# Performance work log

Measured on AMD Instinct MI355X. Metric: run time of the kernel, lower is better.

## Reference

```python
import jax, jax.numpy as jnp
import numpy as np
import math

D_MODEL = 1024
NUM_HEADS = 16
HEAD_DIM = D_MODEL // NUM_HEADS


def _xavier(key, out_f, in_f):
    limit = math.sqrt(6.0 / (in_f + out_f))
    return jax.random.uniform(key, (out_f, in_f), jnp.float32, -limit, limit)


def ternarize(w):
    # abs-mean threshold -> {-1, 0, +1}
    abs_mean = jnp.mean(jnp.abs(w))
    return jnp.where(jnp.abs(w) > abs_mean, jnp.sign(w), jnp.zeros_like(w))


def setup_inputs() -> dict:
    key = jax.random.key(0)
    kq, kk, kv, kwq, kwk, kwv, kwo = jax.random.split(key, 7)
    B, S = 2, 2048
    return {
        "query": jax.random.normal(kq, (B, S, D_MODEL), jnp.float32),
        "key": jax.random.normal(kk, (B, S, D_MODEL), jnp.float32),
        "value": jax.random.normal(kv, (B, S, D_MODEL), jnp.float32),
        "w_q": _xavier(kwq, D_MODEL, D_MODEL),
        "w_k": _xavier(kwk, D_MODEL, D_MODEL),
        "w_v": _xavier(kwv, D_MODEL, D_MODEL),
        "w_o": _xavier(kwo, D_MODEL, D_MODEL),
    }


def reference(query, key, value, w_q, w_k, w_v, w_o):
    B, S, _ = query.shape
    # ternary projections (F.linear: x @ W.T)
    q = query @ ternarize(w_q).T
    k = key @ ternarize(w_k).T
    v = value @ ternarize(w_v).T
    # [B, H, S, Dh]
    q = q.reshape(B, S, NUM_HEADS, HEAD_DIM).transpose(0, 2, 1, 3)
    k = k.reshape(B, -1, NUM_HEADS, HEAD_DIM).transpose(0, 2, 1, 3)
    v = v.reshape(B, -1, NUM_HEADS, HEAD_DIM).transpose(0, 2, 1, 3)
    scores = jnp.einsum("bhqd,bhkd->bhqk", q, k) / math.sqrt(HEAD_DIM)
    probs = jax.nn.softmax(scores, axis=-1)
    out = jnp.einsum("bhqk,bhkd->bhqd", probs, v)
    out = out.transpose(0, 2, 1, 3).reshape(B, S, D_MODEL)
    return out @ ternarize(w_o).T
```

## Files before the change

### kernel.cpp

```cpp
#include <hip/hip_runtime.h>
#include <cstdint>
#include <cstddef>

typedef __bf16 bfloat;
typedef __bf16 bf16x8 __attribute__((ext_vector_type(8)));
typedef __bf16 bf16x4 __attribute__((ext_vector_type(4)));
typedef float  f32x4  __attribute__((ext_vector_type(4)));

static constexpr int D  = 1024;
static constexpr int S  = 2048;
static constexpr int B  = 2;
static constexpr int H  = 16;
static constexpr int DH = 64;
static constexpr int M  = B * S;
static constexpr int WMAT_N = 1024 * 1024;

#define MFMA_BF16(a, b, c) __builtin_amdgcn_mfma_f32_16x16x32_bf16((a), (b), (c), 0, 0, 0)

__device__ __forceinline__ void gl_lds16(const void* g, void* l) {
  __builtin_amdgcn_global_load_lds(
      (const __attribute__((address_space(1))) void*)g,
      (__attribute__((address_space(3))) void*)l, 16, 0, 0);
}

__global__ void absum_kernel(const float* __restrict__ w0, const float* __restrict__ w1,
                             const float* __restrict__ w2, const float* __restrict__ w3,
                             double* __restrict__ sums) {
  int z = blockIdx.y;
  const float* w = (z == 0) ? w0 : (z == 1) ? w1 : (z == 2) ? w2 : w3;
  const float4* w4 = (const float4*)w;
  double s = 0.0;
  for (int i = blockIdx.x * blockDim.x + threadIdx.x; i < (WMAT_N / 4);
       i += gridDim.x * blockDim.x) {
    float4 v = w4[i];
    s += (double)fabsf(v.x) + (double)fabsf(v.y) + (double)fabsf(v.z) + (double)fabsf(v.w);
  }
  for (int off = 1; off < 64; off <<= 1) s += __shfl_xor(s, off, 64);
  __shared__ double ps[4];
  if ((threadIdx.x & 63) == 0) ps[threadIdx.x >> 6] = s;
  __syncthreads();
  if (threadIdx.x == 0) atomicAdd(&sums[z], ps[0] + ps[1] + ps[2] + ps[3]);
}

__global__ void tern_kernel(const float* __restrict__ w0, const float* __restrict__ w1,
                            const float* __restrict__ w2, const float* __restrict__ w3,
                            bfloat* __restrict__ o0, bfloat* __restrict__ o1,
                            bfloat* __restrict__ o2, bfloat* __restrict__ o3,
                            const double* __restrict__ sums) {
  int z = blockIdx.y;
  const float* w = (z == 0) ? w0 : (z == 1) ? w1 : (z == 2) ? w2 : w3;
  bfloat* o = (z == 0) ? o0 : (z == 1) ? o1 : (z == 2) ? o2 : o3;
  double thr = sums[z] * (1.0 / (double)WMAT_N);
  const float4* w4 = (const float4*)w;
  for (int i = blockIdx.x * blockDim.x + threadIdx.x; i < (WMAT_N / 4);
       i += gridDim.x * blockDim.x) {
    float4 v = w4[i];
    bf16x4 r;
    r[0] = (bfloat)(((double)fabsf(v.x) > thr) ? (v.x > 0.f ? 1.f : -1.f) : 0.f);
    r[1] = (bfloat)(((double)fabsf(v.y) > thr) ? (v.y > 0.f ? 1.f : -1.f) : 0.f);
    r[2] = (bfloat)(((double)fabsf(v.z) > thr) ? (v.z > 0.f ? 1.f : -1.f) : 0.f);
    r[3] = (bfloat)(((double)fabsf(v.w) > thr) ? (v.w > 0.f ? 1.f : -1.f) : 0.f);
    *(bf16x4*)&o[(size_t)i * 4] = r;
  }
}

__global__ void splitcvt3_kernel(const float* __restrict__ qx, const float* __restrict__ kx,
                                 const float* __restrict__ vx, bfloat* __restrict__ qhi,
                                 bfloat* __restrict__ qlo, bfloat* __restrict__ khi,
                                 bfloat* __restrict__ klo, bfloat* __restrict__ vhi) {
  int z = blockIdx.y;
  const float* x = (z == 0) ? qx : (z == 1) ? kx : vx;
  bfloat* hi = (z == 0) ? qhi : (z == 1) ? khi : vhi;
  bfloat* lo = (z == 0) ? qlo : (z == 1) ? klo : nullptr;
  const int n4 = M * D / 4;
  const float4* x4 = (const float4*)x;
  for (int i = blockIdx.x * blockDim.x + threadIdx.x; i < n4; i += gridDim.x * blockDim.x) {
    float4 v = x4[i];
    bf16x4 h;
    h[0] = (bfloat)v.x; h[1] = (bfloat)v.y; h[2] = (bfloat)v.z; h[3] = (bfloat)v.w;
    *(bf16x4*)&hi[(size_t)i * 4] = h;
    if (z < 2) {
      bf16x4 l;
      l[0] = (bfloat)(v.x - (float)h[0]);
      l[1] = (bfloat)(v.y - (float)h[1]);
      l[2] = (bfloat)(v.z - (float)h[2]);
      l[3] = (bfloat)(v.w - (float)h[3]);
      *(bf16x4*)&lo[(size_t)i * 4] = l;
    }
  }
}

__global__ __launch_bounds__(256) void transpose_v(const bfloat* __restrict__ in,
                                                   bfloat* __restrict__ out) {
  __shared__ __align__(16) bfloat T[64 * 72];
  const int t = threadIdx.x;
  const int s0 = blockIdx.x * 64, n0 = blockIdx.y * 64, b = blockIdx.z;
#pragma unroll
  for (int p = 0; p < 2; p++) {
    int e = t * 8 + p * 2048;
    int r = e >> 6, cc = e & 63;
    bf16x8 v = *(const bf16x8*)&in[(size_t)(b * S + s0 + r) * D + n0 + cc];
#pragma unroll
    for (int j = 0; j < 8; j++) T[(cc + j) * 72 + r] = v[j];
  }
  __syncthreads();
#pragma unroll
  for (int p = 0; p < 2; p++) {
    int e = t * 8 + p * 2048;
    int f = e >> 6, cc = e & 63;
    bf16x8 v = *(const bf16x8*)&T[f * 72 + cc];
    *(bf16x8*)&out[(size_t)b * D * S + (size_t)(n0 + f) * S + s0 + cc] = v;
  }
}

__global__ __launch_bounds__(256) void qkv_gemm(
    const bfloat* __restrict__ xqh, const bfloat* __restrict__ xql,
    const bfloat* __restrict__ xkh, const bfloat* __restrict__ xkl,
    const bfloat* __restrict__ xvh, const bfloat* __restrict__ wqt,
    const bfloat* __restrict__ wkt, const bfloat* __restrict__ wvt,
    bfloat* __restrict__ qmh, bfloat* __restrict__ qml,
    bfloat* __restrict__ kmh, bfloat* __restrict__ kml, bfloat* __restrict__ vmm) {
  constexpr int K = D;
  constexpr int N = D;
  __shared__ __align__(16) bfloat As0[128 * 32];
  __shared__ __align__(16) bfloat As1[128 * 32];
  __shared__ __align__(16) bfloat Ws[128 * 32];

  const int z = blockIdx.z;
  const bfloat *A0, *A1 = nullptr, *Wm;
  bfloat *Oh, *Ol = nullptr;
  float scale = 1.f;
  bool split;
  if (z == 0) {
    A0 = xqh; A1 = xql; Wm = wqt; Oh = qmh; Ol = qml;
    scale = 0.18033688f;
    split = true;
  } else if (z == 1) {
    A0 = xkh; A1 = xkl; Wm = wkt; Oh = kmh; Ol = kml; split = true;
  } else {
    A0 = xvh; Wm = wvt; Oh = vmm; split = false;
  }

  const int t = threadIdx.x;
  const int w = t >> 6, lane = t & 63;
  const int quad = lane >> 4, l16 = lane & 15;
  const int wm = w >> 1, wn = w & 1;
  const int m0 = blockIdx.y * 128, n0 = blockIdx.x * 128;

  f32x4 acc[4][4] = {};

  const int sr = t >> 2;
  const int sc = (t & 3) * 8;

  const bfloat* pA0a = A0 + (size_t)(m0 + sr) * K + sc;
  const bfloat* pA0b = A0 + (size_t)(m0 + 64 + sr) * K + sc;
  const bfloat* pA1a = split ? A1 + (size_t)(m0 + sr) * K + sc : nullptr;
  const bfloat* pA1b = split ? A1 + (size_t)(m0 + 64 + sr) * K + sc : nullptr;
  const bfloat* pWa = Wm + (size_t)(n0 + sr) * K + sc;
  const bfloat* pWb = Wm + (size_t)(n0 + 64 + sr) * K + sc;

  for (int kk = 0; kk < K; kk += 32) {
    gl_lds16(pA0a + kk, As0 + w * 512);
    gl_lds16(pA0b + kk, As0 + 2048 + w * 512);
    if (split) {
      gl_lds16(pA1a + kk, As1 + w * 512);
      gl_lds16(pA1b + kk, As1 + 2048 + w * 512);
    }
    gl_lds16(pWa + kk, Ws + w * 512);
    gl_lds16(pWb + kk, Ws + 2048 + w * 512);
    __syncthreads();

    bf16x8 bfrag[4], afrag[4];
#pragma unroll
    for (int nt = 0; nt < 4; nt++)
      bfrag[nt] = *(const bf16x8*)&Ws[(wn * 64 + nt * 16 + l16) * 32 + quad * 8];
#pragma unroll
    for (int mt = 0; mt < 4; mt++)
      afrag[mt] = *(const bf16x8*)&As0[(wm * 64 + mt * 16 + l16) * 32 + quad * 8];
#pragma unroll
    for (int mt = 0; mt < 4; mt++)
#pragma unroll
      for (int nt = 0; nt < 4; nt++)
        acc[mt][nt] = MFMA_BF16(afrag[mt], bfrag[nt], acc[mt][nt]);
    if (split) {
#pragma unroll
      for (int mt = 0; mt < 4; mt++)
        afrag[mt] = *(const bf16x8*)&As1[(wm * 64 + mt * 16 + l16) * 32 + quad * 8];
#pragma unroll
      for (int mt = 0; mt < 4; mt++)
#pragma unroll
        for (int nt = 0; nt < 4; nt++)
          acc[mt][nt] = MFMA_BF16(afrag[mt], bfrag[nt], acc[mt][nt]);
    }
    __syncthreads();
  }

#pragma unroll
  for (int mt = 0; mt < 4; mt++) {
#pragma unroll
    for (int nt = 0; nt < 4; nt++) {
      const int row = m0 + wm * 64 + mt * 16 + quad * 4;
      const int col = n0 + wn * 64 + nt * 16 + l16;
#pragma unroll
      for (int rg = 0; rg < 4; rg++) {
        float vv = acc[mt][nt][rg] * scale;
        size_t idx = (size_t)(row + rg) * N + col;
        bfloat hh = (bfloat)vv;
        Oh[idx] = hh;
        if (split) Ol[idx] = (bfloat)(vv - (float)hh);
      }
    }
  }
}

__global__ __launch_bounds__(256) void gemm_wo(const bfloat* __restrict__ A,
                                               const bfloat* __restrict__ Wm,
                                               float* __restrict__ Cf) {
  constexpr int K = D;
  constexpr int N = D;
  __shared__ __align__(16) bfloat As[128 * 32];
  __shared__ __align__(16) bfloat Ws[64 * 32];

  const int t = threadIdx.x;
  const int w = t >> 6, lane = t & 63;
  const int quad = lane >> 4, l16 = lane & 15;
  const int wm = w >> 1, wn = w & 1;
  const int m0 = blockIdx.y * 128, n0 = blockIdx.x * 64;

  f32x4 acc[4][2] = {};

  const int sr = t >> 2;
  const int sc = (t & 3) * 8;
  const bfloat* pAa = A + (size_t)(m0 + sr) * K + sc;
  const bfloat* pAb = A + (size_t)(m0 + 64 + sr) * K + sc;
  const bfloat* pW = Wm + (size_t)(n0 + sr) * K + sc;

  for (int kk = 0; kk < K; kk += 32) {
    gl_lds16(pAa + kk, As + w * 512);
    gl_lds16(pAb + kk, As + 2048 + w * 512);
    gl_lds16(pW + kk, Ws + w * 512);
    __syncthreads();

    bf16x8 bfrag[2], afrag[4];
#pragma unroll
    for (int nt = 0; nt < 2; nt++)
      bfrag[nt] = *(const bf16x8*)&Ws[(wn * 32 + nt * 16 + l16) * 32 + quad * 8];
#pragma unroll
    for (int mt = 0; mt < 4; mt++)
      afrag[mt] = *(const bf16x8*)&As[(wm * 64 + mt * 16 + l16) * 32 + quad * 8];
#pragma unroll
    for (int mt = 0; mt < 4; mt++)
#pragma unroll
      for (int nt = 0; nt < 2; nt++)
        acc[mt][nt] = MFMA_BF16(afrag[mt], bfrag[nt], acc[mt][nt]);
    __syncthreads();
  }

#pragma unroll
  for (int mt = 0; mt < 4; mt++) {
#pragma unroll
    for (int nt = 0; nt < 2; nt++) {
      const int row = m0 + wm * 64 + mt * 16 + quad * 4;
      const int col = n0 + wn * 32 + nt * 16 + l16;
#pragma unroll
      for (int rg = 0; rg < 4; rg++) Cf[(size_t)(row + rg) * N + col] = acc[mt][nt][rg];
    }
  }
}

__global__ __launch_bounds__(256, 4) void flash_kernel(
    const bfloat* __restrict__ qh, const bfloat* __restrict__ ql,
    const bfloat* __restrict__ kh, const bfloat* __restrict__ kl,
    const bfloat* __restrict__ vt, bfloat* __restrict__ outp) {
  __shared__ __align__(16) bfloat Kh[64 * 64];
  __shared__ __align__(16) bfloat Kl[64 * 64];
  __shared__ __align__(16) bfloat Vt[80 * 64];
  __shared__ __align__(16) bfloat Pm[64 * 64];

  const int t = threadIdx.x;
  const int w = t >> 6, lane = t & 63;
  const int quad = lane >> 4, l16 = lane & 15;
  const int b = blockIdx.z, h = blockIdx.y;
  const int q0 = blockIdx.x * 64;
  const size_t base = (size_t)b * S * D + (size_t)h * DH;
  const size_t vbase = (size_t)b * D * S + (size_t)h * DH * S;

  const int ssr = lane >> 3;
  const int spc = lane & 7;

  {
    bf16x4 one = {(bfloat)1.f, (bfloat)1.f, (bfloat)1.f, (bfloat)1.f};
    *(bf16x4*)&Vt[64 * 64 + t * 4] = one;
  }
#pragma unroll
  for (int g = 0; g < 2; g++) {
    int r = w * 16 + g * 8 + ssr;
    int c = spc ^ (r & 7);
    int lo = (w * 16 + g * 8) * 64;
    gl_lds16(qh + base + (size_t)(q0 + r) * D + c * 8, Kh + lo);
    gl_lds16(ql + base + (size_t)(q0 + r) * D + c * 8, Kl + lo);
  }
  __syncthreads();
  bf16x8 ah[2], al[2];
  {
    int row = w * 16 + l16;
#pragma unroll
    for (int s2 = 0; s2 < 2; s2++) {
      ah[s2] = *(const bf16x8*)&Kh[row * 64 + (((s2 * 4 + quad) ^ (row & 7)) * 8)];
      al[s2] = *(const bf16x8*)&Kl[row * 64 + (((s2 * 4 + quad) ^ (row & 7)) * 8)];
    }
  }

  f32x4 Oa[4] = {};
  f32x4 La = {};
  float m_i[4];
#pragma unroll
  for (int i = 0; i < 4; i++) m_i[i] = -3.0e38f;

  for (int k0 = 0; k0 < S; k0 += 64) {
    __syncthreads();
#pragma unroll
    for (int g = 0; g < 2; g++) {
      int r = w * 16 + g * 8 + ssr;
      int c = spc ^ (r & 7);
      int lo = (w * 16 + g * 8) * 64;
      gl_lds16(kh + base + (size_t)(k0 + r) * D + c * 8, Kh + lo);
      gl_lds16(kl + base + (size_t)(k0 + r) * D + c * 8, Kl + lo);
      gl_lds16(vt + vbase + (size_t)r * S + k0 + c * 8, Vt + lo);
    }
    __syncthreads();

    f32x4 sf[4];
#pragma unroll
    for (int nt = 0; nt < 4; nt++) {
      f32x4 acc = {};
      int row = nt * 16 + l16;
#pragma unroll
      for (int s2 = 0; s2 < 2; s2++) {
        bf16x8 bh = *(const bf16x8*)&Kh[row * 64 + (((s2 * 4 + quad) ^ (row & 7)) * 8)];
        bf16x8 bl = *(const bf16x8*)&Kl[row * 64 + (((s2 * 4 + quad) ^ (row & 7)) * 8)];
        acc = MFMA_BF16(ah[s2], bh, acc);
        acc = MFMA_BF16(al[s2], bh, acc);
        acc = MFMA_BF16(ah[s2], bl, acc);
      }
      sf[nt] = acc;
    }

#pragma unroll
    for (int rg = 0; rg < 4; rg++) {
      float mm = fmaxf(fmaxf(sf[0][rg], sf[1][rg]), fmaxf(sf[2][rg], sf[3][rg]));
#pragma unroll
      for (int off = 1; off < 16; off <<= 1) mm = fmaxf(mm, __shfl_xor(mm, off, 64));
      float mnew = fmaxf(m_i[rg], mm);
      float alpha = exp2f(m_i[rg] - mnew);
      m_i[rg] = mnew;
#pragma unroll
      for (int nt = 0; nt < 4; nt++) sf[nt][rg] = exp2f(sf[nt][rg] - mnew);
#pragma unroll
      for (int nt = 0; nt < 4; nt++) Oa[nt][rg] *= alpha;
      La[rg] *= alpha;
    }

#pragma unroll
    for (int nt = 0; nt < 4; nt++)
#pragma unroll
      for (int rg = 0; rg < 4; rg++) {
        int row = w * 16 + quad * 4 + rg;
        int col = nt * 16 + l16;
        Pm[row * 64 + (((col >> 3) ^ (row & 7)) * 8) + (col & 7)] = (bfloat)sf[nt][rg];
      }

    int prow = w * 16 + l16;
#pragma unroll
    for (int s2 = 0; s2 < 2; s2++) {
      bf16x8 pa = *(const bf16x8*)&Pm[prow * 64 + (((s2 * 4 + quad) ^ (prow & 7)) * 8)];
#pragma unroll
      for (int nt = 0; nt < 4; nt++) {
        int vrow = nt * 16 + l16;
        bf16x8 vb = *(const bf16x8*)&Vt[vrow * 64 + (((s2 * 4 + quad) ^ (vrow & 7)) * 8)];
        Oa[nt] = MFMA_BF16(pa, vb, Oa[nt]);
      }
      bf16x8 vb1 = *(const bf16x8*)&Vt[(64 + l16) * 64 + (((s2 * 4 + quad) ^ (l16 & 7)) * 8)];
      La = MFMA_BF16(pa, vb1, La);
    }
  }

#pragma unroll
  for (int rg = 0; rg < 4; rg++) {
    float inv = 1.0f / La[rg];
#pragma unroll
    for (int nt = 0; nt < 4; nt++) {
      outp[base + (size_t)(q0 + w * 16 + quad * 4 + rg) * D + nt * 16 + l16] =
          (bfloat)(Oa[nt][rg] * inv);
    }
  }
}

extern "C" void kernel_launch(void* const* d_in, const int* in_sizes, int n_in,
                              void* d_out, int out_size, void* d_ws, size_t ws_size,
                              hipStream_t stream) {
  const float* q_in = (const float*)d_in[0];
  const float* k_in = (const float*)d_in[1];
  const float* v_in = (const float*)d_in[2];
  const float* wq = (const float*)d_in[3];
  const float* wk = (const float*)d_in[4];
  const float* wv = (const float*)d_in[5];
  const float* wo = (const float*)d_in[6];
  float* outp = (float*)d_out;
  char* ws = (char*)d_ws;

  constexpr size_t WBYTES = (size_t)WMAT_N * 2;
  constexpr size_t XBYTES = (size_t)M * D * 2;
  size_t off = 0;
  double* sums = (double*)(ws + off); off += 256;
  bfloat* wqt = (bfloat*)(ws + off); off += WBYTES;
  bfloat* wkt = (bfloat*)(ws + off); off += WBYTES;
  bfloat* wvt = (bfloat*)(ws + off); off += WBYTES;
  bfloat* wot = (bfloat*)(ws + off); off += WBYTES;
  bfloat* xqh = (bfloat*)(ws + off); off += XBYTES;
  bfloat* xql = (bfloat*)(ws + off); off += XBYTES;
  bfloat* xkh = (bfloat*)(ws + off); off += XBYTES;
  bfloat* xkl = (bfloat*)(ws + off); off += XBYTES;
  bfloat* xvh = (bfloat*)(ws + off); off += XBYTES;
  bfloat* qmh = (bfloat*)(ws + off); off += XBYTES;
  bfloat* qml = (bfloat*)(ws + off); off += XBYTES;
  bfloat* kmh = (bfloat*)(ws + off); off += XBYTES;
  bfloat* kml = (bfloat*)(ws + off); off += XBYTES;
  bfloat* vmm = (bfloat*)(ws + off); off += XBYTES;
  bfloat* attn = xqh;
  bfloat* vtr = xvh;

  hipMemsetAsync(sums, 0, 4 * sizeof(double), stream);
  absum_kernel<<<dim3(128, 4), 256, 0, stream>>>(wq, wk, wv, wo, sums);
  tern_kernel<<<dim3(128, 4), 256, 0, stream>>>(wq, wk, wv, wo, wqt, wkt, wvt, wot, sums);
  splitcvt3_kernel<<<dim3(512, 3), 256, 0, stream>>>(q_in, k_in, v_in, xqh, xql, xkh, xkl, xvh);
  qkv_gemm<<<dim3(D / 128, M / 128, 3), 256, 0, stream>>>(
      xqh, xql, xkh, xkl, xvh, wqt, wkt, wvt, qmh, qml, kmh, kml, vmm);
  transpose_v<<<dim3(S / 64, D / 64, B), 256, 0, stream>>>(vmm, vtr);
  flash_kernel<<<dim3(S / 64, H, B), 256, 0, stream>>>(qmh, qml, kmh, kml, vtr, attn);
  gemm_wo<<<dim3(D / 64, M / 128), 256, 0, stream>>>(attn, wot, outp);
}
```

Baseline: 328.7 us.

## Process 128 query rows per flash block, with DPP row-max and a register ones vector

The flash attention block now covers 128 query rows, two 16-row tiles per wave, so each K/V tile loaded into LDS is reused across twice as many queries. The row-max reduction uses DPP swizzles instead of __shfl_xor, and the row-sum MFMA takes an all-ones operand from a register rather than extra LDS rows. The barrier moves to the end of the loop and launch_bounds drops the occupancy hint. In exchange the grid is half as large (512 blocks) and each thread holds more registers, which may lower occupancy.

Result: slower. 337.0 us (+2.5%).

```diff
diff --git a/kernel.cpp b/kernel.cpp
--- a/kernel.cpp
+++ b/kernel.cpp
@@ -21,6 +21,23 @@
   __builtin_amdgcn_global_load_lds(
       (const __attribute__((address_space(1))) void*)g,
       (__attribute__((address_space(3))) void*)l, 16, 0, 0);
+}
+
+__device__ __forceinline__ float dpp_max16(float x) {
+  float y;
+  y = __builtin_bit_cast(float, __builtin_amdgcn_update_dpp(
+          0, __builtin_bit_cast(int, x), 0xB1, 0xF, 0xF, true));
+  x = fmaxf(x, y);
+  y = __builtin_bit_cast(float, __builtin_amdgcn_update_dpp(
+          0, __builtin_bit_cast(int, x), 0x4E, 0xF, 0xF, true));
+  x = fmaxf(x, y);
+  y = __builtin_bit_cast(float, __builtin_amdgcn_update_dpp(
+          0, __builtin_bit_cast(int, x), 0x141, 0xF, 0xF, true));
+  x = fmaxf(x, y);
+  y = __builtin_bit_cast(float, __builtin_amdgcn_update_dpp(
+          0, __builtin_bit_cast(int, x), 0x140, 0xF, 0xF, true));
+  x = fmaxf(x, y);
+  return x;
 }
 
 __global__ void absum_kernel(const float* __restrict__ w0, const float* __restrict__ w1,
@@ -268,57 +285,66 @@
   }
 }
 
-__global__ __launch_bounds__(256, 4) void flash_kernel(
+__global__ __launch_bounds__(256) void flash_kernel(
     const bfloat* __restrict__ qh, const bfloat* __restrict__ ql,
     const bfloat* __restrict__ kh, const bfloat* __restrict__ kl,
     const bfloat* __restrict__ vt, bfloat* __restrict__ outp) {
   __shared__ __align__(16) bfloat Kh[64 * 64];
   __shared__ __align__(16) bfloat Kl[64 * 64];
-  __shared__ __align__(16) bfloat Vt[80 * 64];
-  __shared__ __align__(16) bfloat Pm[64 * 64];
+  __shared__ __align__(16) bfloat Vt[64 * 64];
+  __shared__ __align__(16) bfloat Pm[128 * 64];
 
   const int t = threadIdx.x;
   const int w = t >> 6, lane = t & 63;
   const int quad = lane >> 4, l16 = lane & 15;
   const int b = blockIdx.z, h = blockIdx.y;
-  const int q0 = blockIdx.x * 64;
+  const int q0 = blockIdx.x * 128;
   const size_t base = (size_t)b * S * D + (size_t)h * DH;
   const size_t vbase = (size_t)b * D * S + (size_t)h * DH * S;
 
   const int ssr = lane >> 3;
   const int spc = lane & 7;
 
-  {
-    bf16x4 one = {(bfloat)1.f, (bfloat)1.f, (bfloat)1.f, (bfloat)1.f};
-    *(bf16x4*)&Vt[64 * 64 + t * 4] = one;
-  }
-#pragma unroll
-  for (int g = 0; g < 2; g++) {
-    int r = w * 16 + g * 8 + ssr;
-    int c = spc ^ (r & 7);
-    int lo = (w * 16 + g * 8) * 64;
-    gl_lds16(qh + base + (size_t)(q0 + r) * D + c * 8, Kh + lo);
-    gl_lds16(ql + base + (size_t)(q0 + r) * D + c * 8, Kl + lo);
-  }
-  __syncthreads();
-  bf16x8 ah[2], al[2];
-  {
-    int row = w * 16 + l16;
-#pragma unroll
-    for (int s2 = 0; s2 < 2; s2++) {
-      ah[s2] = *(const bf16x8*)&Kh[row * 64 + (((s2 * 4 + quad) ^ (row & 7)) * 8)];
-      al[s2] = *(const bf16x8*)&Kl[row * 64 + (((s2 * 4 + quad) ^ (row & 7)) * 8)];
-    }
-  }
-
-  f32x4 Oa[4] = {};
-  f32x4 La = {};
-  float m_i[4];
-#pragma unroll
-  for (int i = 0; i < 4; i++) m_i[i] = -3.0e38f;
+  bf16x8 ones;
+#pragma unroll
+  for (int j = 0; j < 8; j++) ones[j] = (bfloat)1.f;
+
+  bf16x8 ah[2][2], al[2][2];
+#pragma unroll
+  for (int phase = 0; phase < 2; phase++) {
+    const bfloat* src = phase ? ql : qh;
+#pragma unroll
+    for (int g = 0; g < 4; g++) {
+      int r = w * 32 + g * 8 + ssr;
+      int c = spc ^ (r & 7);
+      bfloat* dst = (r < 64) ? (Kh + (w * 32 + g * 8) * 64)
+                             : (Kl + (w * 32 + g * 8 - 64) * 64);
+      gl_lds16(src + base + (size_t)(q0 + r) * D + c * 8, dst);
+    }
+    __syncthreads();
+#pragma unroll
+    for (int rt = 0; rt < 2; rt++) {
+      int row = w * 32 + rt * 16 + l16;
+      const bfloat* buf = (row < 64) ? Kh : Kl;
+      int brow = row & 63;
+#pragma unroll
+      for (int s2 = 0; s2 < 2; s2++) {
+        bf16x8 v = *(const bf16x8*)&buf[brow * 64 + (((s2 * 4 + quad) ^ (row & 7)) * 8)];
+        if (phase) al[rt][s2] = v; else ah[rt][s2] = v;
+      }
+    }
+    __syncthreads();
+  }
+
+  f32x4 Oa[2][4] = {};
+  f32x4 La[2] = {};
+  float m_i[2][4];
+#pragma unroll
+  for (int rt = 0; rt < 2; rt++)
+#pragma unroll
+    for (int i = 0; i < 4; i++) m_i[rt][i] = -3.0e38f;
 
   for (int k0 = 0; k0 < S; k0 += 64) {
-    __syncthreads();
 #pragma unroll
     for (int g = 0; g < 2; g++) {
       int r = w * 16 + g * 8 + ssr;
@@ -330,70 +356,84 @@
     }
     __syncthreads();
 
-    f32x4 sf[4];
+    f32x4 sf[2][4];
 #pragma unroll
     for (int nt = 0; nt < 4; nt++) {
-      f32x4 acc = {};
+      f32x4 a0 = {}, a1 = {};
       int row = nt * 16 + l16;
 #pragma unroll
       for (int s2 = 0; s2 < 2; s2++) {
         bf16x8 bh = *(const bf16x8*)&Kh[row * 64 + (((s2 * 4 + quad) ^ (row & 7)) * 8)];
         bf16x8 bl = *(const bf16x8*)&Kl[row * 64 + (((s2 * 4 + quad) ^ (row & 7)) * 8)];
-        acc = MFMA_BF16(ah[s2], bh, acc);
-        acc = MFMA_BF16(al[s2], bh, acc);
-        acc = MFMA_BF16(ah[s2], bl, acc);
-      }
-      sf[nt] = acc;
-    }
-
-#pragma unroll
-    for (int rg = 0; rg < 4; rg++) {
-      float mm = fmaxf(fmaxf(sf[0][rg], sf[1][rg]), fmaxf(sf[2][rg], sf[3][rg]));
-#pragma unroll
-      for (int off = 1; off < 16; off <<= 1) mm = fmaxf(mm, __shfl_xor(mm, off, 64));
-      float mnew = fmaxf(m_i[rg], mm);
-      float alpha = exp2f(m_i[rg] - mnew);
-      m_i[rg] = mnew;
-#pragma unroll
-      for (int nt = 0; nt < 4; nt++) sf[nt][rg] = exp2f(sf[nt][rg] - mnew);
-#pragma unroll
-      for (int nt = 0; nt < 4; nt++) Oa[nt][rg] *= alpha;
-      La[rg] *= alpha;
-    }
-
-#pragma unroll
-    for (int nt = 0; nt < 4; nt++)
+        a0 = MFMA_BF16(ah[0][s2], bh, a0);
+        a0 = MFMA_BF16(al[0][s2], bh, a0);
+        a0 = MFMA_BF16(ah[0][s2], bl, a0);
+        a1 = MFMA_BF16(ah[1][s2], bh, a1);
+        a1 = MFMA_BF16(al[1][s2], bh, a1);
+        a1 = MFMA_BF16(ah[1][s2], bl, a1);
+      }
+      sf[0][nt] = a0;
+      sf[1][nt] = a1;
+    }
+
+#pragma unroll
+    for (int rt = 0; rt < 2; rt++) {
 #pragma unroll
       for (int rg = 0; rg < 4; rg++) {
-        int row = w * 16 + quad * 4 + rg;
-        int col = nt * 16 + l16;
-        Pm[row * 64 + (((col >> 3) ^ (row & 7)) * 8) + (col & 7)] = (bfloat)sf[nt][rg];
-      }
-
-    int prow = w * 16 + l16;
+        float mm = fmaxf(fmaxf(sf[rt][0][rg], sf[rt][1][rg]),
+                         fmaxf(sf[rt][2][rg], sf[rt][3][rg]));
+        mm = dpp_max16(mm);
+        float mnew = fmaxf(m_i[rt][rg], mm);
+        float alpha = exp2f(m_i[rt][rg] - mnew);
+        m_i[rt][rg] = mnew;
+#pragma unroll
+        for (int nt = 0; nt < 4; nt++) sf[rt][nt][rg] = exp2f(sf[rt][nt][rg] - mnew);
+#pragma unroll
+        for (int nt = 0; nt < 4; nt++) Oa[rt][nt][rg] *= alpha;
+        La[rt][rg] *= alpha;
+      }
+
+#pragma unroll
+      for (int nt = 0; nt < 4; nt++)
+#pragma unroll
+        for (int rg = 0; rg < 4; rg++) {
+          int row = w * 32 + rt * 16 + quad * 4 + rg;
+          int col = nt * 16 + l16;
+          Pm[row * 64 + (((col >> 3) ^ (row & 7)) * 8) + (col & 7)] =
+              (bfloat)sf[rt][nt][rg];
+        }
+    }
+
 #pragma unroll
     for (int s2 = 0; s2 < 2; s2++) {
-      bf16x8 pa = *(const bf16x8*)&Pm[prow * 64 + (((s2 * 4 + quad) ^ (prow & 7)) * 8)];
+      int pr0 = w * 32 + l16;
+      int pr1 = w * 32 + 16 + l16;
+      bf16x8 pa0 = *(const bf16x8*)&Pm[pr0 * 64 + (((s2 * 4 + quad) ^ (pr0 & 7)) * 8)];
+      bf16x8 pa1 = *(const bf16x8*)&Pm[pr1 * 64 + (((s2 * 4 + quad) ^ (pr1 & 7)) * 8)];
 #pragma unroll
       for (int nt = 0; nt < 4; nt++) {
         int vrow = nt * 16 + l16;
         bf16x8 vb = *(const bf16x8*)&Vt[vrow * 64 + (((s2 * 4 + quad) ^ (vrow & 7)) * 8)];
-        Oa[nt] = MFMA_BF16(pa, vb, Oa[nt]);
-      }
-      bf16x8 vb1 = *(const bf16x8*)&Vt[(64 + l16) * 64 + (((s2 * 4 + quad) ^ (l16 & 7)) * 8)];
-      La = MFMA_BF16(pa, vb1, La);
-    }
-  }
-
-#pragma unroll
-  for (int rg = 0; rg < 4; rg++) {
-    float inv = 1.0f / La[rg];
-#pragma unroll
-    for (int nt = 0; nt < 4; nt++) {
-      outp[base + (size_t)(q0 + w * 16 + quad * 4 + rg) * D + nt * 16 + l16] =
-          (bfloat)(Oa[nt][rg] * inv);
-    }
-  }
+        Oa[0][nt] = MFMA_BF16(pa0, vb, Oa[0][nt]);
+        Oa[1][nt] = MFMA_BF16(pa1, vb, Oa[1][nt]);
+      }
+      La[0] = MFMA_BF16(pa0, ones, La[0]);
+      La[1] = MFMA_BF16(pa1, ones, La[1]);
+    }
+    __syncthreads();
+  }
+
+#pragma unroll
+  for (int rt = 0; rt < 2; rt++)
+#pragma unroll
+    for (int rg = 0; rg < 4; rg++) {
+      float inv = 1.0f / La[rt][rg];
+#pragma unroll
+      for (int nt = 0; nt < 4; nt++) {
+        outp[base + (size_t)(q0 + w * 32 + rt * 16 + quad * 4 + rg) * D + nt * 16 + l16] =
+            (bfloat)(Oa[rt][nt][rg] * inv);
+      }
+    }
 }
 
 extern "C" void kernel_launch(void* const* d_in, const int* in_sizes, int n_in,
@@ -437,6 +477,6 @@
   qkv_gemm<<<dim3(D / 128, M / 128, 3), 256, 0, stream>>>(
       xqh, xql, xkh, xkl, xvh, wqt, wkt, wvt, qmh, qml, kmh, kml, vmm);
   transpose_v<<<dim3(S / 64, D / 64, B), 256, 0, stream>>>(vmm, vtr);
-  flash_kernel<<<dim3(S / 64, H, B), 256, 0, stream>>>(qmh, qml, kmh, kml, vtr, attn);
+  flash_kernel<<<dim3(S / 128, H, B), 256, 0, stream>>>(qmh, qml, kmh, kml, vtr, attn);
   gemm_wo<<<dim3(D / 64, M / 128), 256, 0, stream>>>(attn, wot, outp);
 }
```

## Fuse V transpose into QKV GEMM epilogue and transpose flash attention MFMA roles

Applied to the files above, without the earlier changes.

The V projection epilogue now writes its output directly in transposed layout, which removes the separate transpose_v kernel and its extra round trip through global memory. The flash kernel is restructured to compute S^T, with K as the A operand and Q as the B operand. Each lane then owns one query row, so the row max needs only two cross-lane shuffles and P can be stored and output written as packed 4-wide vectors. The ones row in LDS is replaced by a register constant, the barrier moves to the end of the loop, and the launch-bounds occupancy hint is dropped. Risks include strided 8-byte scattered stores in the GEMM epilogue and changed register pressure without the occupancy hint.

After: 301.9 us. 8.2% less time.

```diff
diff --git a/kernel.cpp b/kernel.cpp
--- a/kernel.cpp
+++ b/kernel.cpp
@@ -90,36 +90,13 @@
   }
 }
 
-__global__ __launch_bounds__(256) void transpose_v(const bfloat* __restrict__ in,
-                                                   bfloat* __restrict__ out) {
-  __shared__ __align__(16) bfloat T[64 * 72];
-  const int t = threadIdx.x;
-  const int s0 = blockIdx.x * 64, n0 = blockIdx.y * 64, b = blockIdx.z;
-#pragma unroll
-  for (int p = 0; p < 2; p++) {
-    int e = t * 8 + p * 2048;
-    int r = e >> 6, cc = e & 63;
-    bf16x8 v = *(const bf16x8*)&in[(size_t)(b * S + s0 + r) * D + n0 + cc];
-#pragma unroll
-    for (int j = 0; j < 8; j++) T[(cc + j) * 72 + r] = v[j];
-  }
-  __syncthreads();
-#pragma unroll
-  for (int p = 0; p < 2; p++) {
-    int e = t * 8 + p * 2048;
-    int f = e >> 6, cc = e & 63;
-    bf16x8 v = *(const bf16x8*)&T[f * 72 + cc];
-    *(bf16x8*)&out[(size_t)b * D * S + (size_t)(n0 + f) * S + s0 + cc] = v;
-  }
-}
-
 __global__ __launch_bounds__(256) void qkv_gemm(
     const bfloat* __restrict__ xqh, const bfloat* __restrict__ xql,
     const bfloat* __restrict__ xkh, const bfloat* __restrict__ xkl,
     const bfloat* __restrict__ xvh, const bfloat* __restrict__ wqt,
     const bfloat* __restrict__ wkt, const bfloat* __restrict__ wvt,
     bfloat* __restrict__ qmh, bfloat* __restrict__ qml,
-    bfloat* __restrict__ kmh, bfloat* __restrict__ kml, bfloat* __restrict__ vmm) {
+    bfloat* __restrict__ kmh, bfloat* __restrict__ kml, bfloat* __restrict__ vtr) {
   constexpr int K = D;
   constexpr int N = D;
   __shared__ __align__(16) bfloat As0[128 * 32];
@@ -128,7 +105,7 @@
 
   const int z = blockIdx.z;
   const bfloat *A0, *A1 = nullptr, *Wm;
-  bfloat *Oh, *Ol = nullptr;
+  bfloat *Oh = nullptr, *Ol = nullptr;
   float scale = 1.f;
   bool split;
   if (z == 0) {
@@ -138,7 +115,7 @@
   } else if (z == 1) {
     A0 = xkh; A1 = xkl; Wm = wkt; Oh = kmh; Ol = kml; split = true;
   } else {
-    A0 = xvh; Wm = wvt; Oh = vmm; split = false;
+    A0 = xvh; Wm = wvt; split = false;
   }
 
   const int t = threadIdx.x;
@@ -201,13 +178,21 @@
     for (int nt = 0; nt < 4; nt++) {
       const int row = m0 + wm * 64 + mt * 16 + quad * 4;
       const int col = n0 + wn * 64 + nt * 16 + l16;
-#pragma unroll
-      for (int rg = 0; rg < 4; rg++) {
-        float vv = acc[mt][nt][rg] * scale;
-        size_t idx = (size_t)(row + rg) * N + col;
-        bfloat hh = (bfloat)vv;
-        Oh[idx] = hh;
-        if (split) Ol[idx] = (bfloat)(vv - (float)hh);
+      if (split) {
+#pragma unroll
+        for (int rg = 0; rg < 4; rg++) {
+          float vv = acc[mt][nt][rg] * scale;
+          size_t idx = (size_t)(row + rg) * N + col;
+          bfloat hh = (bfloat)vv;
+          Oh[idx] = hh;
+          Ol[idx] = (bfloat)(vv - (float)hh);
+        }
+      } else {
+        int bb = row >> 11, s = row & (S - 1);
+        bf16x4 pk;
+#pragma unroll
+        for (int rg = 0; rg < 4; rg++) pk[rg] = (bfloat)acc[mt][nt][rg];
+        *(bf16x4*)&vtr[(size_t)bb * D * S + (size_t)col * S + s] = pk;
       }
     }
   }
@@ -268,13 +253,13 @@
   }
 }
 
-__global__ __launch_bounds__(256, 4) void flash_kernel(
+__global__ __launch_bounds__(256) void flash_kernel(
     const bfloat* __restrict__ qh, const bfloat* __restrict__ ql,
     const bfloat* __restrict__ kh, const bfloat* __restrict__ kl,
     const bfloat* __restrict__ vt, bfloat* __restrict__ outp) {
   __shared__ __align__(16) bfloat Kh[64 * 64];
   __shared__ __align__(16) bfloat Kl[64 * 64];
-  __shared__ __align__(16) bfloat Vt[80 * 64];
+  __shared__ __align__(16) bfloat Vt[64 * 64];
   __shared__ __align__(16) bfloat Pm[64 * 64];
 
   const int t = threadIdx.x;
@@ -288,10 +273,10 @@
   const int ssr = lane >> 3;
   const int spc = lane & 7;
 
-  {
-    bf16x4 one = {(bfloat)1.f, (bfloat)1.f, (bfloat)1.f, (bfloat)1.f};
-    *(bf16x4*)&Vt[64 * 64 + t * 4] = one;
-  }
+  bf16x8 ones;
+#pragma unroll
+  for (int j = 0; j < 8; j++) ones[j] = (bfloat)1.f;
+
 #pragma unroll
   for (int g = 0; g < 2; g++) {
     int r = w * 16 + g * 8 + ssr;
@@ -301,24 +286,22 @@
     gl_lds16(ql + base + (size_t)(q0 + r) * D + c * 8, Kl + lo);
   }
   __syncthreads();
-  bf16x8 ah[2], al[2];
+  bf16x8 qhf[2], qlf[2];
   {
     int row = w * 16 + l16;
 #pragma unroll
     for (int s2 = 0; s2 < 2; s2++) {
-      ah[s2] = *(const bf16x8*)&Kh[row * 64 + (((s2 * 4 + quad) ^ (row & 7)) * 8)];
-      al[s2] = *(const bf16x8*)&Kl[row * 64 + (((s2 * 4 + quad) ^ (row & 7)) * 8)];
-    }
-  }
+      qhf[s2] = *(const bf16x8*)&Kh[row * 64 + (((s2 * 4 + quad) ^ (l16 & 7)) * 8)];
+      qlf[s2] = *(const bf16x8*)&Kl[row * 64 + (((s2 * 4 + quad) ^ (l16 & 7)) * 8)];
+    }
+  }
+  __syncthreads();
 
   f32x4 Oa[4] = {};
   f32x4 La = {};
-  float m_i[4];
-#pragma unroll
-  for (int i = 0; i < 4; i++) m_i[i] = -3.0e38f;
+  float m_i = -3.0e38f;
 
   for (int k0 = 0; k0 < S; k0 += 64) {
-    __syncthreads();
 #pragma unroll
     for (int g = 0; g < 2; g++) {
       int r = w * 16 + g * 8 + ssr;
@@ -332,67 +315,70 @@
 
     f32x4 sf[4];
 #pragma unroll
-    for (int nt = 0; nt < 4; nt++) {
-      f32x4 acc = {};
-      int row = nt * 16 + l16;
+    for (int mt = 0; mt < 4; mt++) {
+      f32x4 a = {};
+      int krow = mt * 16 + l16;
 #pragma unroll
       for (int s2 = 0; s2 < 2; s2++) {
-        bf16x8 bh = *(const bf16x8*)&Kh[row * 64 + (((s2 * 4 + quad) ^ (row & 7)) * 8)];
-        bf16x8 bl = *(const bf16x8*)&Kl[row * 64 + (((s2 * 4 + quad) ^ (row & 7)) * 8)];
-        acc = MFMA_BF16(ah[s2], bh, acc);
-        acc = MFMA_BF16(al[s2], bh, acc);
-        acc = MFMA_BF16(ah[s2], bl, acc);
+        bf16x8 bh = *(const bf16x8*)&Kh[krow * 64 + (((s2 * 4 + quad) ^ (l16 & 7)) * 8)];
+        bf16x8 bl = *(const bf16x8*)&Kl[krow * 64 + (((s2 * 4 + quad) ^ (l16 & 7)) * 8)];
+        a = MFMA_BF16(bh, qhf[s2], a);
+        a = MFMA_BF16(bl, qhf[s2], a);
+        a = MFMA_BF16(bh, qlf[s2], a);
       }
-      sf[nt] = acc;
-    }
-
-#pragma unroll
-    for (int rg = 0; rg < 4; rg++) {
-      float mm = fmaxf(fmaxf(sf[0][rg], sf[1][rg]), fmaxf(sf[2][rg], sf[3][rg]));
-#pragma unroll
-      for (int off = 1; off < 16; off <<= 1) mm = fmaxf(mm, __shfl_xor(mm, off, 64));
-      float mnew = fmaxf(m_i[rg], mm);
-      float alpha = exp2f(m_i[rg] - mnew);
-      m_i[rg] = mnew;
-#pragma unroll
-      for (int nt = 0; nt < 4; nt++) sf[nt][rg] = exp2f(sf[nt][rg] - mnew);
-#pragma unroll
-      for (int nt = 0; nt < 4; nt++) Oa[nt][rg] *= alpha;
-      La[rg] *= alpha;
-    }
-
-#pragma unroll
-    for (int nt = 0; nt < 4; nt++)
-#pragma unroll
-      for (int rg = 0; rg < 4; rg++) {
-        int row = w * 16 + quad * 4 + rg;
-        int col = nt * 16 + l16;
-        Pm[row * 64 + (((col >> 3) ^ (row & 7)) * 8) + (col & 7)] = (bfloat)sf[nt][rg];
+      sf[mt] = a;
+    }
+
+    float mm = sf[0][0];
+#pragma unroll
+    for (int mt = 0; mt < 4; mt++)
+#pragma unroll
+      for (int rg = 0; rg < 4; rg++) mm = fmaxf(mm, sf[mt][rg]);
+    mm = fmaxf(mm, __shfl_xor(mm, 16, 64));
+    mm = fmaxf(mm, __shfl_xor(mm, 32, 64));
+    float mnew = fmaxf(m_i, mm);
+    float alpha = exp2f(m_i - mnew);
+    m_i = mnew;
+#pragma unroll
+    for (int mt = 0; mt < 4; mt++)
+#pragma unroll
+      for (int rg = 0; rg < 4; rg++) sf[mt][rg] = exp2f(sf[mt][rg] - mnew);
+#pragma unroll
+    for (int mt = 0; mt < 4; mt++) Oa[mt] *= alpha;
+    La *= alpha;
+
+#pragma unroll
+    for (int mt = 0; mt < 4; mt++) {
+      bf16x4 pk;
+#pragma unroll
+      for (int rg = 0; rg < 4; rg++) pk[rg] = (bfloat)sf[mt][rg];
+      int g16 = (mt * 2 + (quad >> 1)) ^ (l16 & 7);
+      *(bf16x4*)&Pm[(w * 16 + l16) * 64 + g16 * 8 + (quad & 1) * 4] = pk;
+    }
+
+#pragma unroll
+    for (int s2 = 0; s2 < 2; s2++) {
+      bf16x8 pb = *(const bf16x8*)&Pm[(w * 16 + l16) * 64 +
+                                      (((s2 * 4 + quad) ^ (l16 & 7)) * 8)];
+#pragma unroll
+      for (int mt = 0; mt < 4; mt++) {
+        int vrow = mt * 16 + l16;
+        bf16x8 va = *(const bf16x8*)&Vt[vrow * 64 + (((s2 * 4 + quad) ^ (l16 & 7)) * 8)];
+        Oa[mt] = MFMA_BF16(va, pb, Oa[mt]);
       }
-
-    int prow = w * 16 + l16;
-#pragma unroll
-    for (int s2 = 0; s2 < 2; s2++) {
-      bf16x8 pa = *(const bf16x8*)&Pm[prow * 64 + (((s2 * 4 + quad) ^ (prow & 7)) * 8)];
-#pragma unroll
-      for (int nt = 0; nt < 4; nt++) {
-        int vrow = nt * 16 + l16;
-        bf16x8 vb = *(const bf16x8*)&Vt[vrow * 64 + (((s2 * 4 + quad) ^ (vrow & 7)) * 8)];
-        Oa[nt] = MFMA_BF16(pa, vb, Oa[nt]);
-      }
-      bf16x8 vb1 = *(const bf16x8*)&Vt[(64 + l16) * 64 + (((s2 * 4 + quad) ^ (l16 & 7)) * 8)];
-      La = MFMA_BF16(pa, vb1, La);
-    }
-  }
-
-#pragma unroll
-  for (int rg = 0; rg < 4; rg++) {
-    float inv = 1.0f / La[rg];
-#pragma unroll
-    for (int nt = 0; nt < 4; nt++) {
-      outp[base + (size_t)(q0 + w * 16 + quad * 4 + rg) * D + nt * 16 + l16] =
-          (bfloat)(Oa[nt][rg] * inv);
-    }
+      La = MFMA_BF16(ones, pb, La);
+    }
+    __syncthreads();
+  }
+
+  float inv = 1.0f / La[0];
+  const int qrow = q0 + w * 16 + l16;
+#pragma unroll
+  for (int mt = 0; mt < 4; mt++) {
+    bf16x4 ov;
+#pragma unroll
+    for (int rg = 0; rg < 4; rg++) ov[rg] = (bfloat)(Oa[mt][rg] * inv);
+    *(bf16x4*)&outp[base + (size_t)qrow * D + mt * 16 + quad * 4] = ov;
   }
 }
 
@@ -426,17 +412,15 @@
   bfloat* qml = (bfloat*)(ws + off); off += XBYTES;
   bfloat* kmh = (bfloat*)(ws + off); off += XBYTES;
   bfloat* kml = (bfloat*)(ws + off); off += XBYTES;
-  bfloat* vmm = (bfloat*)(ws + off); off += XBYTES;
+  bfloat* vtr = (bfloat*)(ws + off); off += XBYTES;
   bfloat* attn = xqh;
-  bfloat* vtr = xvh;
 
   hipMemsetAsync(sums, 0, 4 * sizeof(double), stream);
   absum_kernel<<<dim3(128, 4), 256, 0, stream>>>(wq, wk, wv, wo, sums);
   tern_kernel<<<dim3(128, 4), 256, 0, stream>>>(wq, wk, wv, wo, wqt, wkt, wvt, wot, sums);
   splitcvt3_kernel<<<dim3(512, 3), 256, 0, stream>>>(q_in, k_in, v_in, xqh, xql, xkh, xkl, xvh);
   qkv_gemm<<<dim3(D / 128, M / 128, 3), 256, 0, stream>>>(
-      xqh, xql, xkh, xkl, xvh, wqt, wkt, wvt, qmh, qml, kmh, kml, vmm);
-  transpose_v<<<dim3(S / 64, D / 64, B), 256, 0, stream>>>(vmm, vtr);
+      xqh, xql, xkh, xkl, xvh, wqt, wkt, wvt, qmh, qml, kmh, kml, vtr);
   flash_kernel<<<dim3(S / 64, H, B), 256, 0, stream>>>(qmh, qml, kmh, kml, vtr, attn);
   gemm_wo<<<dim3(D / 64, M / 128), 256, 0, stream>>>(attn, wot, outp);
 }
```
